# Kernel optimization log

Hardware: AMD Instinct MI355X
Metric: run time of the kernel (lower is better)

The kernel has to match this reference:

```python
import jax, jax.numpy as jnp
import numpy as np

B, LQ, LIM = 4, 640, 1296
D_MODEL, NHEAD, DFF, MAX_DIST = 768, 12, 3072, 100
DK = D_MODEL // NHEAD
EPS = 1e-5


def _layer_norm(x, g, b):
    mu = jnp.mean(x, axis=-1, keepdims=True)
    var = jnp.mean(jnp.square(x - mu), axis=-1, keepdims=True)
    return (x - mu) * jax.lax.rsqrt(var + EPS) * g + b


def setup_inputs() -> dict:
    key = jax.random.key(0)
    ks = jax.random.split(key, 24)
    s = 0.02
    inp = {
        "docqa": jax.random.normal(ks[0], (B, LQ, D_MODEL), jnp.float32),
        "im_tokens": jax.random.normal(ks[1], (B, LIM, D_MODEL), jnp.float32),
        "docqa_x": jax.random.randint(ks[2], (B, LQ), 0, 1000, jnp.int32),
        "docqa_y": jax.random.randint(ks[3], (B, LQ), 0, 1000, jnp.int32),
        "im_tokens_x": jax.random.randint(ks[4], (B, LIM), 0, 1000, jnp.int32),
        "im_tokens_y": jax.random.randint(ks[5], (B, LIM), 0, 1000, jnp.int32),
        # attention projection params
        "Wq": jax.random.normal(ks[6], (D_MODEL, D_MODEL), jnp.float32) * s,
        "bq": jnp.zeros((D_MODEL,), jnp.float32),
        "Wk": jax.random.normal(ks[7], (D_MODEL, D_MODEL), jnp.float32) * s,
        "bk": jnp.zeros((D_MODEL,), jnp.float32),
        "Wv": jax.random.normal(ks[8], (D_MODEL, D_MODEL), jnp.float32) * s,
        "bv": jnp.zeros((D_MODEL,), jnp.float32),
        "Wo": jax.random.normal(ks[9], (D_MODEL, D_MODEL), jnp.float32) * s,
        "bo": jnp.zeros((D_MODEL,), jnp.float32),
        # relative position bias tables: (2*max_dist+1, nhead) per axis
        "bias_x": jax.random.normal(ks[10], (2 * MAX_DIST + 1, NHEAD), jnp.float32) * s,
        "bias_y": jax.random.normal(ks[11], (2 * MAX_DIST + 1, NHEAD), jnp.float32) * s,
        # FFN
        "W1": jax.random.normal(ks[12], (D_MODEL, DFF), jnp.float32) * s,
        "b1": jnp.zeros((DFF,), jnp.float32),
        "W2": jax.random.normal(ks[13], (DFF, D_MODEL), jnp.float32) * s,
        "b2": jnp.zeros((D_MODEL,), jnp.float32),
        # LayerNorms
        "g1": jnp.ones((D_MODEL,), jnp.float32),
        "be1": jnp.zeros((D_MODEL,), jnp.float32),
        "g2": jnp.ones((D_MODEL,), jnp.float32),
        "be2": jnp.zeros((D_MODEL,), jnp.float32),
    }
    return inp


def reference(docqa, im_tokens, docqa_x, docqa_y, im_tokens_x, im_tokens_y,
              Wq, bq, Wk, bk, Wv, bv, Wo, bo, bias_x, bias_y,
              W1, b1, W2, b2, g1, be1, g2, be2):
    # keys/values attend over concatenated image tokens + docqa tokens
    full = jnp.concatenate([im_tokens, docqa], axis=1)            # (B, Lk, D)
    full_x = jnp.concatenate([im_tokens_x, docqa_x], axis=1)      # (B, Lk)
    full_y = jnp.concatenate([im_tokens_y, docqa_y], axis=1)

    q = (docqa @ Wq + bq).reshape(B, LQ, NHEAD, DK)               # (B,Lq,H,Dk)
    k = (full @ Wk + bk).reshape(B, LQ + LIM, NHEAD, DK)
    v = (full @ Wv + bv).reshape(B, LQ + LIM, NHEAD, DK)

    scores = jnp.einsum("bqhd,bkhd->bhqk", q, k) / jnp.sqrt(jnp.float32(DK))

    # relative-position bias, clamped to [-max_dist, max_dist]
    rel_x = jnp.clip(docqa_x[:, :, None] - full_x[:, None, :], -MAX_DIST, MAX_DIST) + MAX_DIST
    rel_y = jnp.clip(docqa_y[:, :, None] - full_y[:, None, :], -MAX_DIST, MAX_DIST) + MAX_DIST
    pos_bias = bias_x[rel_x] + bias_y[rel_y]                      # (B,Lq,Lk,H)
    scores = scores + jnp.transpose(pos_bias, (0, 3, 1, 2))       # (B,H,Lq,Lk)

    attn = jax.nn.softmax(scores, axis=-1)
    ctx = jnp.einsum("bhqk,bkhd->bqhd", attn, v).reshape(B, LQ, D_MODEL)
    attn_out = ctx @ Wo + bo

    # residual + norm + FFN + residual + norm (dropout=0 in eval)
    src = _layer_norm(docqa + attn_out, g1, be1)
    ffn = jnp.maximum(src @ W1 + b1, 0.0) @ W2 + b2
    src = _layer_norm(src + ffn, g2, be2)
    return src
```

## Files before the change

### kernel.cpp

```cpp
#include <hip/hip_runtime.h>
#include <hip/hip_bf16.h>

constexpr int B      = 4;
constexpr int LQ     = 640;
constexpr int LIM    = 1296;
constexpr int LK     = LQ + LIM;
constexpr int DM     = 768;
constexpr int NHEAD  = 12;
constexpr int DK     = 64;
constexpr int DFF    = 3072;
constexpr int MAXD   = 100;
constexpr int M_DOC  = B * LQ;
constexpr int M_FULL = B * LK;
constexpr size_t ML_CNT = (size_t)B * NHEAD * LQ;

typedef __attribute__((ext_vector_type(8))) short bf16x8_t;
typedef __attribute__((ext_vector_type(4))) float f32x4_t;

__device__ __forceinline__ float b2f(__hip_bfloat16 x) { return __bfloat162float(x); }

__device__ __forceinline__ float ldf(const void* p, size_t i, int f32flag) {
    return f32flag ? ((const float*)p)[i]
                   : b2f(((const __hip_bfloat16*)p)[i]);
}

__device__ __forceinline__ void gl_lds16(const void* g, void* l) {
    __builtin_amdgcn_global_load_lds(
        (const __attribute__((address_space(1))) unsigned int*)g,
        (__attribute__((address_space(3))) unsigned int*)l, 16, 0, 0);
}

__global__ __launch_bounds__(256)
void prep_conv_kernel(const void* __restrict__ g1, int* __restrict__ flagp,
                      const void* __restrict__ im, const void* __restrict__ docqa,
                      const int* __restrict__ dqx, const int* __restrict__ dqy,
                      const int* __restrict__ imx, const int* __restrict__ imy,
                      __hip_bfloat16* __restrict__ fullA,
                      int* __restrict__ cx, int* __restrict__ cy)
{
    const bool f32 = ((*(const unsigned*)g1) & 0xFFFFu) == 0u;
    if (blockIdx.x == 0 && threadIdx.x == 0) *flagp = f32 ? 1 : 0;

    const int gid = blockIdx.x * 256 + threadIdx.x;
    if (gid < B * LK) {
        int b = gid / LK, l = gid - b * LK;
        cx[gid] = (l < LIM) ? imx[b * LIM + l] : dqx[b * LQ + l - LIM];
        cy[gid] = (l < LIM) ? imy[b * LIM + l] : dqy[b * LQ + l - LIM];
    }

    if (gid >= M_FULL * (DM / 8)) return;
    const int row = gid / (DM / 8);
    const int col = (gid - row * (DM / 8)) * 8;
    const int b   = row / LK;
    const int l   = row - b * LK;
    const size_t srow = (l < LIM) ? ((size_t)(b * LIM + l)) * DM
                                  : ((size_t)(b * LQ + (l - LIM))) * DM;
    const void* src = (l < LIM) ? im : docqa;
    union { bf16x8_t v; __hip_bfloat16 h[8]; } pk;
    if (f32) {
        const float4* fp = (const float4*)((const float*)src + srow + col);
        float4 a = fp[0], c = fp[1];
        pk.h[0] = __float2bfloat16(a.x); pk.h[1] = __float2bfloat16(a.y);
        pk.h[2] = __float2bfloat16(a.z); pk.h[3] = __float2bfloat16(a.w);
        pk.h[4] = __float2bfloat16(c.x); pk.h[5] = __float2bfloat16(c.y);
        pk.h[6] = __float2bfloat16(c.z); pk.h[7] = __float2bfloat16(c.w);
    } else {
        pk.v = *(const bf16x8_t*)((const __hip_bfloat16*)src + srow + col);
    }
    *(bf16x8_t*)(fullA + (size_t)row * DM + col) = pk.v;
}

__device__ __forceinline__ void wtrans_tile(const void* W, __hip_bfloat16* Wt,
                                            int f32, int K, int N, int n0, int k0,
                                            __hip_bfloat16 (*t)[33])
{
    const int tx = threadIdx.x & 31, ty = threadIdx.x >> 5;
#pragma unroll
    for (int j = 0; j < 4; ++j) {
        int k = ty + j * 8;
        t[k][tx] = __float2bfloat16(ldf(W, (size_t)(k0 + k) * N + n0 + tx, f32));
    }
    __syncthreads();
#pragma unroll
    for (int j = 0; j < 4; ++j) {
        int n = ty + j * 8;
        Wt[(size_t)(n0 + n) * K + k0 + tx] = t[tx][n];
    }
}

__global__ __launch_bounds__(256)
void wtrans3_kernel(const void* __restrict__ Wq, const void* __restrict__ Wk,
                    const void* __restrict__ Wv, __hip_bfloat16* __restrict__ Wt3,
                    const int* __restrict__ flagp)
{
    __shared__ __hip_bfloat16 t[32][33];
    const int f32 = *flagp;
    const int wid = blockIdx.x / 576;
    const int tt  = blockIdx.x % 576;
    const void* W = (wid == 0) ? Wq : (wid == 1) ? Wk : Wv;
    wtrans_tile(W, Wt3 + (size_t)wid * DM * DM, f32, DM, DM,
                (tt % 24) * 32, (tt / 24) * 32, t);
}

__global__ __launch_bounds__(256)
void wtransO_kernel(const void* __restrict__ Wo, __hip_bfloat16* __restrict__ WtO,
                    const int* __restrict__ flagp)
{
    __shared__ __hip_bfloat16 t[32][33];
    const int f32 = *flagp;
    const int tt  = blockIdx.x;
    wtrans_tile(Wo, WtO, f32, DM, DM, (tt % 24) * 32, (tt / 24) * 32, t);
}

__global__ __launch_bounds__(256)
void wtransW_kernel(const void* __restrict__ W1, const void* __restrict__ W2,
                    __hip_bfloat16* __restrict__ W1t, __hip_bfloat16* __restrict__ W2t,
                    const int* __restrict__ flagp)
{
    __shared__ __hip_bfloat16 t[32][33];
    const int f32 = *flagp;
    int bx = blockIdx.x;
    const bool second = bx >= 2304;
    const void* W = second ? W2 : W1;
    __hip_bfloat16* dst = second ? W2t : W1t;
    const int K = second ? DFF : DM;
    const int N = second ? DM : DFF;
    const int tt = second ? bx - 2304 : bx;
    const int nt = N / 32;
    wtrans_tile(W, dst, f32, K, N, (tt % nt) * 32, (tt / nt) * 32, t);
}

__global__ __launch_bounds__(256)
void qkv_gemm(const __hip_bfloat16* __restrict__ fullA,
              const __hip_bfloat16* __restrict__ Wt3,
              const void* __restrict__ bq,
              const void* __restrict__ bk,
              const void* __restrict__ bv,
              __hip_bfloat16* __restrict__ qout,
              __hip_bfloat16* __restrict__ kb,
              __hip_bfloat16* __restrict__ vtb,
              const int* __restrict__ flagp)
{
    __shared__ __hip_bfloat16 Als[128 * 32];
    __shared__ __hip_bfloat16 Bls[128 * 32];

    const int f32  = *flagp;
    const int tid  = threadIdx.x;
    const int lane = tid & 63;
    const int wave = tid >> 6;
    const int quad = lane >> 4;
    const int c16  = lane & 15;
    const int n0   = blockIdx.x * 128;
    const int m0   = blockIdx.y * 128;
    const int wm   = (wave >> 1) * 64;
    const int wn   = (wave & 1) * 64;
    constexpr int K = DM;

    f32x4_t acc[4][4] = {};

    for (int k0 = 0; k0 < K; k0 += 32) {
#pragma unroll
        for (int p = 0; p < 2; ++p) {
            const int lin = p * 64 + lane;
            int row = wave * 32 + (lin >> 2);
            int gr  = m0 + row; if (gr > M_FULL - 1) gr = M_FULL - 1;
            gl_lds16(fullA + (size_t)gr * K + k0 + (lin & 3) * 8,
                     Als + wave * 1024 + p * 512);
        }
#pragma unroll
        for (int p = 0; p < 2; ++p) {
            const int lin = p * 64 + lane;
            const int row = wave * 32 + (lin >> 2);
            gl_lds16(Wt3 + (size_t)(n0 + row) * K + k0 + (lin & 3) * 8,
                     Bls + wave * 1024 + p * 512);
        }
        __syncthreads();

        bf16x8_t af[4], bfr[4];
#pragma unroll
        for (int i = 0; i < 4; ++i)
            af[i] = *(const bf16x8_t*)(Als + (wm + i * 16 + c16) * 32 + quad * 8);
#pragma unroll
        for (int j = 0; j < 4; ++j)
            bfr[j] = *(const bf16x8_t*)(Bls + (wn + j * 16 + c16) * 32 + quad * 8);
#pragma unroll
        for (int i = 0; i < 4; ++i)
#pragma unroll
            for (int j = 0; j < 4; ++j)
                acc[i][j] = __builtin_amdgcn_mfma_f32_16x16x32_bf16(af[i], bfr[j], acc[i][j], 0, 0, 0);
        __syncthreads();
    }

    const int seg = n0 / DM;
    const void* bptr = (seg == 0) ? bq : (seg == 1) ? bk : bv;
#pragma unroll
    for (int j = 0; j < 4; ++j) {
        const int col  = n0 + wn + j * 16 + c16;
        const int ncol = col - seg * DM;
        const float bj = ldf(bptr, ncol, f32);
        if (seg == 2) {
            const int h = ncol >> 6, d = ncol & 63;
#pragma unroll
            for (int i = 0; i < 4; ++i) {
                const int rowb = m0 + wm + i * 16 + quad * 4;
                const int bb0  = rowb / LK;
                const int l0   = rowb - bb0 * LK;
                if (l0 + 3 < LK && rowb + 3 < M_FULL) {
                    union { ushort4 u4; __hip_bfloat16 hh[4]; } pk;
#pragma unroll
                    for (int r = 0; r < 4; ++r)
                        pk.hh[r] = __float2bfloat16(acc[i][j][r] + bj);
                    *(ushort4*)(vtb + ((size_t)((bb0 * NHEAD + h) * DK + d)) * LK + l0) = pk.u4;
                } else {
#pragma unroll
                    for (int r = 0; r < 4; ++r) {
                        const int row = rowb + r;
                        if (row < M_FULL) {
                            int bb = row / LK, l = row - bb * LK;
                            vtb[((size_t)((bb * NHEAD + h) * DK + d)) * LK + l] =
                                __float2bfloat16(acc[i][j][r] + bj);
                        }
                    }
                }
            }
        } else {
            const float scl = (seg == 0) ? 0.125f : 1.f;
#pragma unroll
            for (int i = 0; i < 4; ++i) {
                const int rowb = m0 + wm + i * 16 + quad * 4;
#pragma unroll
                for (int r = 0; r < 4; ++r) {
                    const int row = rowb + r;
                    if (row < M_FULL) {
                        __hip_bfloat16 hv = __float2bfloat16((acc[i][j][r] + bj) * scl);
                        if (seg == 1) kb[(size_t)row * DM + ncol] = hv;
                        else {
                            int bb = row / LK, l = row - bb * LK;
                            if (l >= LIM)
                                qout[(size_t)(bb * LQ + (l - LIM)) * DM + ncol] = hv;
                        }
                    }
                }
            }
        }
    }
}

__global__ __launch_bounds__(256)
void mfma_gemm_relu(const __hip_bfloat16* __restrict__ Abf,
                    const __hip_bfloat16* __restrict__ Wt,
                    const void* __restrict__ bias,
                    __hip_bfloat16* __restrict__ Cc,
                    const int* __restrict__ flagp,
                    int M, int N, int K)
{
    __shared__ __hip_bfloat16 Als[128 * 32];
    __shared__ __hip_bfloat16 Bls[128 * 32];

    const int f32  = *flagp;
    const int tid  = threadIdx.x;
    const int lane = tid & 63;
    const int wave = tid >> 6;
    const int quad = lane >> 4;
    const int c16  = lane & 15;
    const int n0   = blockIdx.x * 128;
    const int m0   = blockIdx.y * 128;
    const int wm   = (wave >> 1) * 64;
    const int wn   = (wave & 1) * 64;

    f32x4_t acc[4][4] = {};

    for (int k0 = 0; k0 < K; k0 += 32) {
#pragma unroll
        for (int p = 0; p < 2; ++p) {
            const int lin = p * 64 + lane;
            int row = wave * 32 + (lin >> 2);
            int gr  = m0 + row; if (gr > M - 1) gr = M - 1;
            gl_lds16(Abf + (size_t)gr * K + k0 + (lin & 3) * 8, Als + wave * 1024 + p * 512);
        }
#pragma unroll
        for (int p = 0; p < 2; ++p) {
            const int lin = p * 64 + lane;
            const int row = wave * 32 + (lin >> 2);
            gl_lds16(Wt + (size_t)(n0 + row) * K + k0 + (lin & 3) * 8,
                     Bls + wave * 1024 + p * 512);
        }
        __syncthreads();

        bf16x8_t af[4], bfr[4];
#pragma unroll
        for (int i = 0; i < 4; ++i)
            af[i] = *(const bf16x8_t*)(Als + (wm + i * 16 + c16) * 32 + quad * 8);
#pragma unroll
        for (int j = 0; j < 4; ++j)
            bfr[j] = *(const bf16x8_t*)(Bls + (wn + j * 16 + c16) * 32 + quad * 8);
#pragma unroll
        for (int i = 0; i < 4; ++i)
#pragma unroll
            for (int j = 0; j < 4; ++j)
                acc[i][j] = __builtin_amdgcn_mfma_f32_16x16x32_bf16(af[i], bfr[j], acc[i][j], 0, 0, 0);
        __syncthreads();
    }

#pragma unroll
    for (int j = 0; j < 4; ++j) {
        const int col = n0 + wn + j * 16 + c16;
        const float bj = ldf(bias, col, f32);
#pragma unroll
        for (int i = 0; i < 4; ++i) {
            const int rowb = m0 + wm + i * 16 + quad * 4;
#pragma unroll
            for (int r = 0; r < 4; ++r) {
                const int row = rowb + r;
                if (row < M) {
                    float v = fmaxf(acc[i][j][r] + bj, 0.f);
                    Cc[(size_t)row * N + col] = __float2bfloat16(v);
                }
            }
        }
    }
}

__global__ __launch_bounds__(256)
void sk_gemm(const __hip_bfloat16* __restrict__ Abf,
             const __hip_bfloat16* __restrict__ Wt,
             float* __restrict__ Cc,
             int M, int N, int K, int S)
{
    __shared__ __hip_bfloat16 Als[128 * 32];
    __shared__ __hip_bfloat16 Bls[128 * 32];

    const int tid  = threadIdx.x;
    const int lane = tid & 63;
    const int wave = tid >> 6;
    const int quad = lane >> 4;
    const int c16  = lane & 15;
    const int n0   = blockIdx.x * 128;
    const int m0   = blockIdx.y * 128;
    const int wm   = (wave >> 1) * 64;
    const int wn   = (wave & 1) * 64;
    const int kchunk = K / S;
    const int kbeg = blockIdx.z * kchunk;

    f32x4_t acc[4][4] = {};

    for (int k0 = kbeg; k0 < kbeg + kchunk; k0 += 32) {
#pragma unroll
        for (int p = 0; p < 2; ++p) {
            const int lin = p * 64 + lane;
            int row = wave * 32 + (lin >> 2);
            int gr  = m0 + row; if (gr > M - 1) gr = M - 1;
            gl_lds16(Abf + (size_t)gr * K + k0 + (lin & 3) * 8, Als + wave * 1024 + p * 512);
        }
#pragma unroll
        for (int p = 0; p < 2; ++p) {
            const int lin = p * 64 + lane;
            const int row = wave * 32 + (lin >> 2);
            gl_lds16(Wt + (size_t)(n0 + row) * K + k0 + (lin & 3) * 8,
                     Bls + wave * 1024 + p * 512);
        }
        __syncthreads();

        bf16x8_t af[4], bfr[4];
#pragma unroll
        for (int i = 0; i < 4; ++i)
            af[i] = *(const bf16x8_t*)(Als + (wm + i * 16 + c16) * 32 + quad * 8);
#pragma unroll
        for (int j = 0; j < 4; ++j)
            bfr[j] = *(const bf16x8_t*)(Bls + (wn + j * 16 + c16) * 32 + quad * 8);
#pragma unroll
        for (int i = 0; i < 4; ++i)
#pragma unroll
            for (int j = 0; j < 4; ++j)
                acc[i][j] = __builtin_amdgcn_mfma_f32_16x16x32_bf16(af[i], bfr[j], acc[i][j], 0, 0, 0);
        __syncthreads();
    }

#pragma unroll
    for (int j = 0; j < 4; ++j) {
        const int col = n0 + wn + j * 16 + c16;
#pragma unroll
        for (int i = 0; i < 4; ++i) {
            const int rowb = m0 + wm + i * 16 + quad * 4;
#pragma unroll
            for (int r = 0; r < 4; ++r) {
                const int row = rowb + r;
                if (row < M) atomicAdd(&Cc[(size_t)row * N + col], acc[i][j][r]);
            }
        }
    }
}

__global__ __launch_bounds__(256)
void attn_part_kernel(const __hip_bfloat16* __restrict__ Qb,
                      const __hip_bfloat16* __restrict__ Kb,
                      const __hip_bfloat16* __restrict__ Vtb,
                      const int* __restrict__ cx, const int* __restrict__ cy,
                      const void* __restrict__ bias_x,
                      const void* __restrict__ bias_y,
                      __hip_bfloat16* __restrict__ p0,
                      __hip_bfloat16* __restrict__ p1,
                      float* __restrict__ mlbase,
                      const int* __restrict__ flagp)
{
    constexpr int QT = 64, KT = 64;
    constexpr int QROW = 72;
    __shared__ __hip_bfloat16 Ps[QT * QROW];
    __shared__ float bxs[2 * MAXD + 1], bys[2 * MAXD + 1];

    const int f32  = *flagp;
    const int tid  = threadIdx.x;
    const int lane = tid & 63;
    const int wave = tid >> 6;
    const int quad = lane >> 4;
    const int c16  = lane & 15;

    const int id   = blockIdx.x;
    const int bh   = id % 48;
    const int rest = id / 48;
    const int s    = rest & 1;
    const int q0   = (rest >> 1) * QT;
    const int b    = bh / NHEAD;
    const int h    = bh - b * NHEAD;
    const int kbeg = s * 1024;
    const int kend = s ? LK : 1024;

    __hip_bfloat16* Op = s ? p1 : p0;
    float* mp = mlbase + (size_t)s * 2 * ML_CNT;
    float* lp = mp + ML_CNT;

    for (int i = tid; i < 2 * MAXD + 1; i += 256) {
        bxs[i] = ldf(bias_x, (size_t)i * NHEAD + h, f32);
        bys[i] = ldf(bias_y, (size_t)i * NHEAD + h, f32);
    }

    const __hip_bfloat16* qrow = Qb + ((size_t)(b * LQ + q0 + wave * 16 + c16)) * DM + h * DK;
    const bf16x8_t aq0 = *(const bf16x8_t*)(qrow + quad * 8);
    const bf16x8_t aq1 = *(const bf16x8_t*)(qrow + 32 + quad * 8);
    int qx[4], qy[4];
#pragma unroll
    for (int r = 0; r < 4; ++r) {
        const int qi = b * LK + LIM + q0 + wave * 16 + quad * 4 + r;
        qx[r] = cx[qi]; qy[r] = cy[qi];
    }
    const __hip_bfloat16* vrow = Vtb + ((size_t)((b * NHEAD + h) * DK)) * LK;

    __syncthreads();

    f32x4_t O[4] = {};
    float m_r[4], l_r[4];
#pragma unroll
    for (int r = 0; r < 4; ++r) { m_r[r] = -1e30f; l_r[r] = 0.f; }

    for (int k0 = kbeg; k0 < kend; k0 += KT) {
        f32x4_t S[4];
#pragma unroll
        for (int jn = 0; jn < 4; ++jn) {
            int krow = k0 + jn * 16 + c16; if (krow > LK - 1) krow = LK - 1;
            const __hip_bfloat16* kr = Kb + ((size_t)(b * LK + krow)) * DM + h * DK;
            bf16x8_t bk0 = *(const bf16x8_t*)(kr + quad * 8);
            bf16x8_t bk1 = *(const bf16x8_t*)(kr + 32 + quad * 8);
            f32x4_t acc = {0.f, 0.f, 0.f, 0.f};
            acc = __builtin_amdgcn_mfma_f32_16x16x32_bf16(aq0, bk0, acc, 0, 0, 0);
            acc = __builtin_amdgcn_mfma_f32_16x16x32_bf16(aq1, bk1, acc, 0, 0, 0);
            S[jn] = acc;
        }
#pragma unroll
        for (int jn = 0; jn < 4; ++jn) {
            const int kg = k0 + jn * 16 + c16;
            const bool ok = kg < LK;
            const int kgc = ok ? kg : LK - 1;
            const int kx = cx[b * LK + kgc], ky = cy[b * LK + kgc];
#pragma unroll
            for (int r = 0; r < 4; ++r) {
                int rx = min(max(qx[r] - kx, -MAXD), MAXD) + MAXD;
                int ry = min(max(qy[r] - ky, -MAXD), MAXD) + MAXD;
                float v = S[jn][r] + bxs[rx] + bys[ry];
                S[jn][r] = ok ? v : -1e30f;
            }
        }
        float alpha[4];
#pragma unroll
        for (int r = 0; r < 4; ++r) {
            float mx = fmaxf(fmaxf(S[0][r], S[1][r]), fmaxf(S[2][r], S[3][r]));
            mx = fmaxf(mx, __shfl_xor(mx, 1));
            mx = fmaxf(mx, __shfl_xor(mx, 2));
            mx = fmaxf(mx, __shfl_xor(mx, 4));
            mx = fmaxf(mx, __shfl_xor(mx, 8));
            const float mt = fmaxf(m_r[r], mx);
            const float al = __expf(m_r[r] - mt);
            float sum = 0.f;
#pragma unroll
            for (int jn = 0; jn < 4; ++jn) {
                float p = __expf(S[jn][r] - mt);
                S[jn][r] = p;
                sum += p;
            }
            sum += __shfl_xor(sum, 1);
            sum += __shfl_xor(sum, 2);
            sum += __shfl_xor(sum, 4);
            sum += __shfl_xor(sum, 8);
            m_r[r] = mt;
            l_r[r] = l_r[r] * al + sum;
            alpha[r] = al;
        }
#pragma unroll
        for (int jn = 0; jn < 4; ++jn)
#pragma unroll
            for (int r = 0; r < 4; ++r)
                Ps[(wave * 16 + quad * 4 + r) * QROW + jn * 16 + c16] = __float2bfloat16(S[jn][r]);
#pragma unroll
        for (int jd = 0; jd < 4; ++jd)
#pragma unroll
            for (int r = 0; r < 4; ++r) O[jd][r] *= alpha[r];
        bf16x8_t ap0 = *(const bf16x8_t*)(Ps + (wave * 16 + c16) * QROW + quad * 8);
        bf16x8_t ap1 = *(const bf16x8_t*)(Ps + (wave * 16 + c16) * QROW + 32 + quad * 8);
        int kc0 = k0 + quad * 8;      if (kc0 > LK - 8) kc0 = LK - 8;
        int kc1 = k0 + 32 + quad * 8; if (kc1 > LK - 8) kc1 = LK - 8;
#pragma unroll
        for (int jd = 0; jd < 4; ++jd) {
            const __hip_bfloat16* vr = vrow + (size_t)(jd * 16 + c16) * LK;
            bf16x8_t bv0 = *(const bf16x8_t*)(vr + kc0);
            bf16x8_t bv1 = *(const bf16x8_t*)(vr + kc1);
            O[jd] = __builtin_amdgcn_mfma_f32_16x16x32_bf16(ap0, bv0, O[jd], 0, 0, 0);
            O[jd] = __builtin_amdgcn_mfma_f32_16x16x32_bf16(ap1, bv1, O[jd], 0, 0, 0);
        }
    }

#pragma unroll
    for (int r = 0; r < 4; ++r) {
        const int ql = wave * 16 + quad * 4 + r;
        const size_t grow = (size_t)(b * LQ + q0 + ql);
#pragma unroll
        for (int jd = 0; jd < 4; ++jd)
            Op[grow * DM + h * DK + jd * 16 + c16] = __float2bfloat16(O[jd][r]);
        if (c16 == 0) {
            size_t mli = ((size_t)b * NHEAD + h) * LQ + q0 + ql;
            mp[mli] = m_r[r];
            lp[mli] = l_r[r];
        }
    }
}

__global__ __launch_bounds__(256)
void attn_merge_kernel(const __hip_bfloat16* __restrict__ p0,
                       const __hip_bfloat16* __restrict__ p1,
                       const float* __restrict__ mlbase,
                       __hip_bfloat16* __restrict__ ctx,
                       float* __restrict__ aof)
{
    const int row = blockIdx.x;
    const int b = row / LQ, q = row - b * LQ;
    const int tid = threadIdx.x;
#pragma unroll
    for (int i = 0; i < 3; ++i) {
        const int c = tid + i * 256;
        const int h = c >> 6;
        const size_t mli = ((size_t)b * NHEAD + h) * LQ + q;
        const float m0 = mlbase[mli],              l0 = mlbase[ML_CNT + mli];
        const float m1 = mlbase[2 * ML_CNT + mli], l1 = mlbase[3 * ML_CNT + mli];
        const float mm = fmaxf(m0, m1);
        const float w0 = __expf(m0 - mm), w1 = __expf(m1 - mm);
        const float denom = l0 * w0 + l1 * w1;
        const size_t idx = (size_t)row * DM + c;
        const float v = (b2f(p0[idx]) * w0 + b2f(p1[idx]) * w1) / denom;
        ctx[idx] = __float2bfloat16(v);
        aof[idx] = 0.f;
    }
}

template<int MODE>
__global__ __launch_bounds__(256)
void ln_kernel(const void* __restrict__ Xin,
               const __hip_bfloat16* __restrict__ Xb,
               const float* __restrict__ Xf2f,
               const void* __restrict__ bias2,
               const void* __restrict__ g,
               const void* __restrict__ be,
               __hip_bfloat16* __restrict__ outb,
               void* __restrict__ outv,
               float* __restrict__ zbuf,
               const int* __restrict__ flagp)
{
    __shared__ float red1[256], red2[256];
    const int f32 = *flagp;
    const int row = blockIdx.x;
    const int tid = threadIdx.x;

    float x[3];
#pragma unroll
    for (int i = 0; i < 3; ++i) {
        int c = tid + i * 256;
        size_t idx = (size_t)row * DM + c;
        float a  = (MODE == 0) ? ldf(Xin, idx, f32) : b2f(Xb[idx]);
        x[i] = a + Xf2f[idx] + ldf(bias2, c, f32);
    }
    float s1 = x[0] + x[1] + x[2];
    float s2 = x[0] * x[0] + x[1] * x[1] + x[2] * x[2];
    red1[tid] = s1;
    red2[tid] = s2;
    __syncthreads();
    for (int off = 128; off > 0; off >>= 1) {
        if (tid < off) {
            red1[tid] += red1[tid + off];
            red2[tid] += red2[tid + off];
        }
        __syncthreads();
    }
    float mu   = red1[0] * (1.f / DM);
    float var  = red2[0] * (1.f / DM) - mu * mu;
    float rstd = rsqrtf(var + 1e-5f);
#pragma unroll
    for (int i = 0; i < 3; ++i) {
        int c = tid + i * 256;
        size_t idx = (size_t)row * DM + c;
        float v = (x[i] - mu) * rstd * ldf(g, c, f32) + ldf(be, c, f32);
        if (MODE == 0) {
            outb[idx] = __float2bfloat16(v);
            zbuf[idx] = 0.f;
        } else {
            if (f32) ((float*)outv)[idx] = v;
            else     ((__hip_bfloat16*)outv)[idx] = __float2bfloat16(v);
        }
    }
}

extern "C" void kernel_launch(void* const* d_in, const int* in_sizes, int n_in,
                              void* d_out, int out_size, void* d_ws, size_t ws_size,
                              hipStream_t stream)
{
    const void* docqa = d_in[0];
    const void* im    = d_in[1];
    const int* dqx = (const int*)d_in[2];
    const int* dqy = (const int*)d_in[3];
    const int* imx = (const int*)d_in[4];
    const int* imy = (const int*)d_in[5];
    const void* Wq = d_in[6];
    const void* bq = d_in[7];
    const void* Wk = d_in[8];
    const void* bk = d_in[9];
    const void* Wv = d_in[10];
    const void* bv = d_in[11];
    const void* Wo = d_in[12];
    const void* bo = d_in[13];
    const void* bias_x = d_in[14];
    const void* bias_y = d_in[15];
    const void* W1 = d_in[16];
    const void* b1 = d_in[17];
    const void* W2 = d_in[18];
    const void* b2 = d_in[19];
    const void* g1  = d_in[20];
    const void* be1 = d_in[21];
    const void* g2  = d_in[22];
    const void* be2 = d_in[23];

    char* w = (char*)d_ws;
    int*            flagp = (int*)w;
    __hip_bfloat16* qR  = (__hip_bfloat16*)(w + 256);
    __hip_bfloat16* kb  = qR + (size_t)M_DOC  * DM;
    __hip_bfloat16* vtb = kb + (size_t)M_FULL * DM;
    __hip_bfloat16* cb  = vtb + (size_t)M_FULL * DM;
    char* cbB = (char*)cb;
    char* r1B = (char*)qR;

    __hip_bfloat16* fullA = cb;
    __hip_bfloat16* Wt3  = qR;
    int*            cxp  = (int*)(r1B + 3538944);
    int*            cyp  = cxp + (size_t)B * LK;
    __hip_bfloat16* WtO  = qR;
    __hip_bfloat16* qout = (__hip_bfloat16*)d_out;
    __hip_bfloat16* p0   = cb;
    __hip_bfloat16* p1   = (__hip_bfloat16*)(cbB + 3932160);
    float*          mlb  = (float*)(cbB + 7864320);
    __hip_bfloat16* ctx  = cb;
    __hip_bfloat16* src1 = cb;
    float*          fof  = (float*)(cbB + 3932160);
    float*          aof  = (float*)vtb;
    __hip_bfloat16* W1t  = vtb;
    __hip_bfloat16* W2t  = vtb + (size_t)DFF * DM;
    __hip_bfloat16* mid  = qR;

    dim3 blk(256);

    prep_conv_kernel<<<dim3((M_FULL * (DM / 8) + 255) / 256), blk, 0, stream>>>(
        g1, flagp, im, docqa, dqx, dqy, imx, imy, fullA, cxp, cyp);
    wtrans3_kernel<<<dim3(3 * 576), blk, 0, stream>>>(Wq, Wk, Wv, Wt3, flagp);
    qkv_gemm<<<dim3(3 * DM / 128, (M_FULL + 127) / 128), blk, 0, stream>>>(
        fullA, Wt3, bq, bk, bv, qout, kb, vtb, flagp);
    attn_part_kernel<<<dim3(48 * 20), blk, 0, stream>>>(
        qout, kb, vtb, cxp, cyp, bias_x, bias_y, p0, p1, mlb, flagp);
    attn_merge_kernel<<<dim3(M_DOC), blk, 0, stream>>>(p0, p1, mlb, ctx, aof);
    wtransO_kernel<<<dim3(576), blk, 0, stream>>>(Wo, WtO, flagp);
    sk_gemm<<<dim3(DM / 128, M_DOC / 128, 4), blk, 0, stream>>>(
        ctx, WtO, aof, M_DOC, DM, DM, 4);
    ln_kernel<0><<<dim3(M_DOC), blk, 0, stream>>>(
        docqa, nullptr, aof, bo, g1, be1, src1, nullptr, fof, flagp);
    wtransW_kernel<<<dim3(2 * 2304), blk, 0, stream>>>(W1, W2, W1t, W2t, flagp);
    mfma_gemm_relu<<<dim3(DFF / 128, M_DOC / 128), blk, 0, stream>>>(
        src1, W1t, b1, mid, flagp, M_DOC, DFF, DM);
    sk_gemm<<<dim3(DM / 128, M_DOC / 128, 4), blk, 0, stream>>>(
        mid, W2t, fof, M_DOC, DM, DFF, 4);
    ln_kernel<1><<<dim3(M_DOC), blk, 0, stream>>>(
        nullptr, src1, fof, b2, g2, be2, nullptr, d_out, nullptr, flagp);
}
```

Baseline: 420.4 us.

## Stage Q, K and V tiles in swizzled LDS via direct global-to-LDS loads

The attention kernel now copies Q once, and K and V tiles on every iteration, into XOR-swizzled shared memory using a global-to-LDS helper. All four waves then read their MFMA operands from LDS instead of each wave fetching the same K/V rows from global memory. This cuts redundant global traffic, but it adds two barriers per K tile and does not double-buffer the tiles, so load latency is no longer hidden behind compute.

```diff
diff --git a/kernel.cpp b/kernel.cpp
--- a/kernel.cpp
+++ b/kernel.cpp
@@ -405,6 +405,9 @@
 {
     constexpr int QT = 64, KT = 64;
     constexpr int QROW = 72;
+    __shared__ __hip_bfloat16 Qs[QT * DK];
+    __shared__ __hip_bfloat16 Ks[KT * DK];
+    __shared__ __hip_bfloat16 Vs[DK * KT];
     __shared__ __hip_bfloat16 Ps[QT * QROW];
     __shared__ float bxs[2 * MAXD + 1], bys[2 * MAXD + 1];
 
@@ -434,32 +437,65 @@
         bys[i] = ldf(bias_y, (size_t)i * NHEAD + h, f32);
     }
 
-    const __hip_bfloat16* qrow = Qb + ((size_t)(b * LQ + q0 + wave * 16 + c16)) * DM + h * DK;
-    const bf16x8_t aq0 = *(const bf16x8_t*)(qrow + quad * 8);
-    const bf16x8_t aq1 = *(const bf16x8_t*)(qrow + 32 + quad * 8);
+    const __hip_bfloat16* kbase = Kb + ((size_t)(b * LK)) * DM + h * DK;
+    const __hip_bfloat16* vbase = Vtb + ((size_t)((b * NHEAD + h) * DK)) * LK;
+    const __hip_bfloat16* qbase = Qb + ((size_t)(b * LQ + q0)) * DM + h * DK;
+
+    {
+        const int rsub = lane >> 3;
+        const int cg0  = (lane & 7) ^ (rsub & 7);
+#pragma unroll
+        for (int p = 0; p < 2; ++p) {
+            const int rl = wave * 16 + p * 8 + rsub;
+            gl_lds16(qbase + (size_t)rl * DM + cg0 * 8, Qs + (wave * 16 + p * 8) * DK);
+        }
+    }
+
     int qx[4], qy[4];
 #pragma unroll
     for (int r = 0; r < 4; ++r) {
         const int qi = b * LK + LIM + q0 + wave * 16 + quad * 4 + r;
         qx[r] = cx[qi]; qy[r] = cy[qi];
     }
-    const __hip_bfloat16* vrow = Vtb + ((size_t)((b * NHEAD + h) * DK)) * LK;
 
     __syncthreads();
+
+    const int sw  = c16 & 7;
+    const int cA0 = (quad ^ sw) * 8;
+    const int cA1 = ((quad + 4) ^ sw) * 8;
+    const int rQ  = wave * 16 + c16;
+    const bf16x8_t aq0 = *(const bf16x8_t*)(Qs + rQ * DK + cA0);
+    const bf16x8_t aq1 = *(const bf16x8_t*)(Qs + rQ * DK + cA1);
 
     f32x4_t O[4] = {};
     float m_r[4], l_r[4];
 #pragma unroll
     for (int r = 0; r < 4; ++r) { m_r[r] = -1e30f; l_r[r] = 0.f; }
 
+    const int rsub = lane >> 3;
+    const int cgl  = (lane & 7) ^ (rsub & 7);
+
     for (int k0 = kbeg; k0 < kend; k0 += KT) {
+#pragma unroll
+        for (int p = 0; p < 2; ++p) {
+            const int rl = wave * 16 + p * 8 + rsub;
+            int gr = k0 + rl; if (gr > LK - 1) gr = LK - 1;
+            gl_lds16(kbase + (size_t)gr * DM + cgl * 8, Ks + (wave * 16 + p * 8) * DK);
+        }
+#pragma unroll
+        for (int p = 0; p < 2; ++p) {
+            const int dl = wave * 16 + p * 8 + rsub;
+            int kks = k0 + cgl * 8; if (kks > LK - 8) kks = LK - 8;
+            gl_lds16(vbase + (size_t)dl * LK + kks, Vs + (wave * 16 + p * 8) * KT);
+        }
+        __syncthreads();
+
         f32x4_t S[4];
 #pragma unroll
         for (int jn = 0; jn < 4; ++jn) {
-            int krow = k0 + jn * 16 + c16; if (krow > LK - 1) krow = LK - 1;
-            const __hip_bfloat16* kr = Kb + ((size_t)(b * LK + krow)) * DM + h * DK;
-            bf16x8_t bk0 = *(const bf16x8_t*)(kr + quad * 8);
-            bf16x8_t bk1 = *(const bf16x8_t*)(kr + 32 + quad * 8);
+            const int rK = jn * 16 + c16;
+            bf16x8_t bk0 = *(const bf16x8_t*)(Ks + rK * DK + cA0);
+            bf16x8_t bk1 = *(const bf16x8_t*)(Ks + rK * DK + cA1);
             f32x4_t acc = {0.f, 0.f, 0.f, 0.f};
             acc = __builtin_amdgcn_mfma_f32_16x16x32_bf16(aq0, bk0, acc, 0, 0, 0);
             acc = __builtin_amdgcn_mfma_f32_16x16x32_bf16(aq1, bk1, acc, 0, 0, 0);
@@ -515,16 +551,15 @@
             for (int r = 0; r < 4; ++r) O[jd][r] *= alpha[r];
         bf16x8_t ap0 = *(const bf16x8_t*)(Ps + (wave * 16 + c16) * QROW + quad * 8);
         bf16x8_t ap1 = *(const bf16x8_t*)(Ps + (wave * 16 + c16) * QROW + 32 + quad * 8);
-        int kc0 = k0 + quad * 8;      if (kc0 > LK - 8) kc0 = LK - 8;
-        int kc1 = k0 + 32 + quad * 8; if (kc1 > LK - 8) kc1 = LK - 8;
 #pragma unroll
         for (int jd = 0; jd < 4; ++jd) {
-            const __hip_bfloat16* vr = vrow + (size_t)(jd * 16 + c16) * LK;
-            bf16x8_t bv0 = *(const bf16x8_t*)(vr + kc0);
-            bf16x8_t bv1 = *(const bf16x8_t*)(vr + kc1);
+            const int rV = jd * 16 + c16;
+            bf16x8_t bv0 = *(const bf16x8_t*)(Vs + rV * KT + cA0);
+            bf16x8_t bv1 = *(const bf16x8_t*)(Vs + rV * KT + cA1);
             O[jd] = __builtin_amdgcn_mfma_f32_16x16x32_bf16(ap0, bv0, O[jd], 0, 0, 0);
             O[jd] = __builtin_amdgcn_mfma_f32_16x16x32_bf16(ap1, bv1, O[jd], 0, 0, 0);
         }
+        __syncthreads();
     }
 
 #pragma unroll
```

New measurement: 402.3 us. 1.04x faster.
